# Performance work log

Hardware: AMD Instinct MI355X
Metric: run time of the kernel (lower is better)

Reference implementation:

```python
import jax, jax.numpy as jnp
import numpy as np

L, H, T, C, OUT, B = 8, 16, 2048, 1024, 1024, 4
DH = C // H
EPS = 1e-5


def _sincos_pos_embed(embed_dim, n):
    omega = np.arange(embed_dim // 2, dtype=np.float64) / (embed_dim / 2.0)
    omega = 1.0 / 10000 ** omega
    out = np.einsum('m,d->md', np.arange(n, dtype=np.float64), omega)
    return np.concatenate([np.sin(out), np.cos(out)], axis=1).astype(np.float32)


def setup_inputs() -> dict:
    key = jax.random.key(0)
    ks = jax.random.split(key, 12)
    s = 0.02  # torch init std
    n = lambda k, sh: jax.random.normal(k, sh, jnp.float32) * s
    zc = jnp.zeros((L, C), jnp.float32)
    return {
        'seq': jax.random.normal(ks[0], (B, T, C), jnp.float32),
        'pos_embed': jnp.asarray(_sincos_pos_embed(C, T))[None],  # [1,T,C]
        'Wq': n(ks[1], (L, C, C)), 'bq': zc,
        'Wk': n(ks[2], (L, C, C)), 'bk': zc,
        'Wv': n(ks[3], (L, C, C)), 'bv': zc,
        'Wo': n(ks[4], (L, C, C)), 'bo': zc,
        'ln1_w': jnp.ones((L, C), jnp.float32), 'ln1_b': zc,
        'ln2_w': jnp.ones((L, C), jnp.float32), 'ln2_b': zc,
        'W1': n(ks[5], (L, 4 * C, C)), 'b1': jnp.zeros((L, 4 * C), jnp.float32),
        'W2': n(ks[6], (L, C, 4 * C)), 'b2': zc,
        'lnf_w': jnp.ones((C,), jnp.float32), 'lnf_b': jnp.zeros((C,), jnp.float32),
        'Whead': n(ks[7], (OUT, C)),
    }


def _ln(x, w, b):
    mu = jnp.mean(x, -1, keepdims=True)
    var = jnp.mean(jnp.square(x - mu), -1, keepdims=True)
    return (x - mu) * jax.lax.rsqrt(var + EPS) * w + b


def _block(x, p):
    (Wq, bq, Wk, bk, Wv, bv, Wo, bo, l1w, l1b, l2w, l2b, W1, b1, W2, b2) = p
    b_, t_, c_ = x.shape
    h = _ln(x, l1w, l1b)
    q = (h @ Wq.T + bq).reshape(b_, t_, H, DH)
    k = (h @ Wk.T + bk).reshape(b_, t_, H, DH)
    v = (h @ Wv.T + bv).reshape(b_, t_, H, DH)
    # NOTE: source mask buffer is all ones -> no masking (full softmax)
    att = jnp.einsum('bqhd,bkhd->bhqk', q, k) * (1.0 / np.sqrt(DH))
    att = jax.nn.softmax(att, axis=-1)
    y = jnp.einsum('bhqk,bkhd->bqhd', att, v).reshape(b_, t_, c_)
    x = x + y @ Wo.T + bo
    h2 = _ln(x, l2w, l2b)
    x = x + jax.nn.gelu(h2 @ W1.T + b1, approximate=False) @ W2.T + b2
    return x, None


def reference(seq, pos_embed, Wq, bq, Wk, bk, Wv, bv, Wo, bo,
              ln1_w, ln1_b, ln2_w, ln2_b, W1, b1, W2, b2,
              lnf_w, lnf_b, Whead):
    t = seq.shape[1]
    x = seq + pos_embed[:, -t:, :]  # embedding dropout is identity at eval
    params = (Wq, bq, Wk, bk, Wv, bv, Wo, bo, ln1_w, ln1_b, ln2_w, ln2_b, W1, b1, W2, b2)
    x, _ = jax.lax.scan(_block, x, params)
    x = _ln(x, lnf_w, lnf_b)
    return x @ Whead.T
```

## Files before the change

kernel.cpp:

```cpp
#include <hip/hip_runtime.h>
#include <hip/hip_bf16.h>


#define LAYERS 8
#define NH 16
#define TT 2048
#define CC 1024
#define NB 4
#define MR (NB*TT)
#define LN_EPS 1e-5f

typedef __bf16 bf16_t;
typedef __attribute__((ext_vector_type(8))) __bf16 bf16x8;
typedef __attribute__((ext_vector_type(4))) __bf16 bf16x4;
typedef __attribute__((ext_vector_type(4))) float f32x4;
typedef __attribute__((ext_vector_type(8))) short s16x8;

__device__ inline f32x4 mfma16x16x32(bf16x8 a, bf16x8 b, f32x4 c) {
    return __builtin_amdgcn_mfma_f32_16x16x32_bf16(a, b, c, 0, 0, 0);
}

__device__ inline void gload_lds16(const void* g, void* lds) {
    __builtin_amdgcn_global_load_lds((const __attribute__((address_space(1))) void*)g,
                                     (__attribute__((address_space(3))) void*)lds, 16, 0, 0);
}


__global__ __launch_bounds__(256) void add_pos_k(const float* __restrict__ s,
                                                 const float* __restrict__ p,
                                                 float* __restrict__ x) {
    int i = blockIdx.x * 256 + threadIdx.x;
    float4 a = ((const float4*)s)[i];
    float4 b = ((const float4*)p)[i & ((TT * CC / 4) - 1)];
    ((float4*)x)[i] = make_float4(a.x + b.x, a.y + b.y, a.z + b.z, a.w + b.w);
}

__global__ __launch_bounds__(256) void f32_to_bf16_k(const float* __restrict__ s,
                                                     bf16_t* __restrict__ d, int n4) {
    int i = blockIdx.x * 256 + threadIdx.x;
    if (i < n4) {
        float4 v = ((const float4*)s)[i];
        bf16x4 o;
        o[0] = (bf16_t)v.x; o[1] = (bf16_t)v.y; o[2] = (bf16_t)v.z; o[3] = (bf16_t)v.w;
        ((bf16x4*)d)[i] = o;
    }
}

__global__ __launch_bounds__(256) void convert_layer_k(
        const float* __restrict__ Wq, const float* __restrict__ Wk,
        const float* __restrict__ Wv, const float* __restrict__ Wo,
        const float* __restrict__ W1, const float* __restrict__ W2,
        const float* __restrict__ bq, const float* __restrict__ bk,
        const float* __restrict__ bv,
        bf16_t* __restrict__ wqkvb, bf16_t* __restrict__ wob,
        bf16_t* __restrict__ w1b, bf16_t* __restrict__ w2b,
        float* __restrict__ bqkv) {
    const int i = blockIdx.x * 256 + threadIdx.x;
    if (i < 3145728) {
        const float4* s4;
        bf16_t* dst;
        int off;
        if (i < 262144)       { s4 = (const float4*)Wq + i;             dst = wqkvb; off = i; }
        else if (i < 524288)  { s4 = (const float4*)Wk + (i - 262144);  dst = wqkvb; off = i; }
        else if (i < 786432)  { s4 = (const float4*)Wv + (i - 524288);  dst = wqkvb; off = i; }
        else if (i < 1048576) { s4 = (const float4*)Wo + (i - 786432);  dst = wob;   off = i - 786432; }
        else if (i < 2097152) { s4 = (const float4*)W1 + (i - 1048576); dst = w1b;   off = i - 1048576; }
        else                  { s4 = (const float4*)W2 + (i - 2097152); dst = w2b;   off = i - 2097152; }
        float4 v = *s4;
        bf16x4 o;
        o[0] = (bf16_t)v.x; o[1] = (bf16_t)v.y; o[2] = (bf16_t)v.z; o[3] = (bf16_t)v.w;
        ((bf16x4*)dst)[off] = o;
    } else if (i < 3146496) {
        const int j = i - 3145728;
        const float* b = (j < 256) ? bq : (j < 512 ? bk : bv);
        ((float4*)bqkv)[j] = ((const float4*)b)[j & 255];
    }
}


__global__ __launch_bounds__(256) void ln_rows_k(const float* __restrict__ x,
                                                 const float* __restrict__ wgt,
                                                 const float* __restrict__ bgt,
                                                 bf16_t* __restrict__ out) {
    const int row = blockIdx.x * 4 + (threadIdx.x >> 6);
    const int l = threadIdx.x & 63;
    const float* xr = x + (size_t)row * CC;
    float4 v[4];
    float s = 0.f, sq = 0.f;
#pragma unroll
    for (int j = 0; j < 4; j++) {
        v[j] = *(const float4*)&xr[j * 256 + l * 4];
        s  += v[j].x + v[j].y + v[j].z + v[j].w;
        sq += v[j].x * v[j].x + v[j].y * v[j].y + v[j].z * v[j].z + v[j].w * v[j].w;
    }
#pragma unroll
    for (int m = 1; m < 64; m <<= 1) { s += __shfl_xor(s, m); sq += __shfl_xor(sq, m); }
    const float mu = s * (1.f / CC);
    const float rstd = rsqrtf(sq * (1.f / CC) - mu * mu + LN_EPS);
#pragma unroll
    for (int j = 0; j < 4; j++) {
        const int c0 = j * 256 + l * 4;
        const float4 wv = *(const float4*)&wgt[c0];
        const float4 bv = *(const float4*)&bgt[c0];
        bf16x4 o;
        o[0] = (bf16_t)((v[j].x - mu) * rstd * wv.x + bv.x);
        o[1] = (bf16_t)((v[j].y - mu) * rstd * wv.y + bv.y);
        o[2] = (bf16_t)((v[j].z - mu) * rstd * wv.z + bv.z);
        o[3] = (bf16_t)((v[j].w - mu) * rstd * wv.w + bv.w);
        *(bf16x4*)&out[(size_t)row * CC + c0] = o;
    }
}


#define EPI_BF16 0
#define EPI_GELU 1
#define EPI_RES  2
#define EPI_F32  3

template <int EPI>
__global__ __launch_bounds__(256) void gemm_bt(const bf16_t* __restrict__ A,
                                               const bf16_t* __restrict__ Bw,
                                               const float* __restrict__ bias,
                                               float* __restrict__ resid,
                                               bf16_t* __restrict__ obf,
                                               float* __restrict__ of32,
                                               int N, int K, int nbn) {
    __shared__ __align__(16) bf16_t As[128 * 32];
    __shared__ __align__(16) bf16_t Bs[128 * 32];
    const int nwg = gridDim.x;
    const int id = blockIdx.x;
    const int swz = (id & 7) * (nwg >> 3) + (id >> 3);
    const int bn = swz % nbn, bm = swz / nbn;
    const int t = threadIdx.x, w = t >> 6, l = t & 63;
    const int wm = (w >> 1) << 6, wn = (w & 1) << 6;
    const int fr = l & 15, fg = l >> 4;
    const int srow = l >> 2, scol = (l & 3) * 8;
    f32x4 acc[4][4] = {};
    for (int k0 = 0; k0 < K; k0 += 32) {
#pragma unroll
        for (int it = 0; it < 2; ++it) {
            const int rr = it * 64 + w * 16;
            gload_lds16(A  + (size_t)(bm * 128 + rr + srow) * K + k0 + scol, &As[rr * 32]);
            gload_lds16(Bw + (size_t)(bn * 128 + rr + srow) * K + k0 + scol, &Bs[rr * 32]);
        }
        __syncthreads();
        bf16x8 af[4], bfv[4];
#pragma unroll
        for (int i = 0; i < 4; i++) af[i]  = *(const bf16x8*)&As[(wm + i * 16 + fr) * 32 + fg * 8];
#pragma unroll
        for (int j = 0; j < 4; j++) bfv[j] = *(const bf16x8*)&Bs[(wn + j * 16 + fr) * 32 + fg * 8];
#pragma unroll
        for (int i = 0; i < 4; i++)
#pragma unroll
            for (int j = 0; j < 4; j++)
                acc[i][j] = mfma16x16x32(af[i], bfv[j], acc[i][j]);
        __syncthreads();
    }
#pragma unroll
    for (int i = 0; i < 4; i++) {
#pragma unroll
        for (int j = 0; j < 4; j++) {
            const int col = bn * 128 + wn + j * 16 + fr;
            float bv = 0.f;
            if constexpr (EPI != EPI_F32) bv = bias[col];
#pragma unroll
            for (int rg = 0; rg < 4; ++rg) {
                const int row = bm * 128 + wm + i * 16 + fg * 4 + rg;
                float v = acc[i][j][rg] + bv;
                if constexpr (EPI == EPI_BF16) {
                    obf[(size_t)row * N + col] = (bf16_t)v;
                } else if constexpr (EPI == EPI_GELU) {
                    v = 0.5f * v * (1.0f + erff(v * 0.70710678118f));
                    obf[(size_t)row * N + col] = (bf16_t)v;
                } else if constexpr (EPI == EPI_RES) {
                    resid[(size_t)row * CC + col] += v;
                } else {
                    of32[(size_t)row * N + col] = v;
                }
            }
        }
    }
}


__global__ __launch_bounds__(256, 2) void attn_k(const bf16_t* __restrict__ qkv,
                                                 bf16_t* __restrict__ y) {
    __shared__ __align__(16) bf16_t Ks[64 * 64];
    __shared__ __align__(16) bf16_t Vt[64 * 64];
    __shared__ __align__(16) bf16_t Ps[4 * 16 * 64];
    const int id = blockIdx.x;
    const int swz = (id & 7) * 256 + (id >> 3);
    const int qt = swz & 31, bh = swz >> 5;
    const int b = bh >> 4, h = bh & 15;
    const int t = threadIdx.x, w = t >> 6, l = t & 63;
    const int fr = l & 15, fg = l >> 4;
    const int q0 = qt * 64 + w * 16;
    const size_t bT = (size_t)b * TT;
    const float c2 = 0.125f * 1.44269504f;

    bf16x8 qf[2];
    {
        const size_t qoff = (bT + q0 + fr) * 3072 + h * 64 + fg * 8;
        qf[0] = *(const bf16x8*)&qkv[qoff];
        qf[1] = *(const bf16x8*)&qkv[qoff + 32];
    }
    float m[4] = {-1e30f, -1e30f, -1e30f, -1e30f};
    float lse[4] = {0.f, 0.f, 0.f, 0.f};
    f32x4 oacc[4] = {};

    const int srow = t >> 2;
    const int c8a = (t & 3) * 8;
    const int ksw = (srow & 7) << 4;
    char* KsB = (char*)Ks;
    char* VtB = (char*)Vt;
    char* PsB = (char*)Ps + w * 2048;

    s16x8 kr0, kr1, vr0, vr1;
    auto preload = [&](int kv0) {
        const size_t roff = (bT + kv0 + srow) * 3072 + h * 64;
        kr0 = *(const s16x8*)&qkv[roff + 1024 + c8a];
        kr1 = *(const s16x8*)&qkv[roff + 1024 + c8a + 32];
        vr0 = *(const s16x8*)&qkv[roff + 2048 + c8a];
        vr1 = *(const s16x8*)&qkv[roff + 2048 + c8a + 32];
    };
    preload(0);

    for (int kv0 = 0; kv0 < TT; kv0 += 64) {
        __syncthreads();
#pragma unroll
        for (int half = 0; half < 2; ++half) {
            const s16x8 kr = half ? kr1 : kr0;
            const s16x8 vr = half ? vr1 : vr0;
            const int c8 = c8a + half * 32;
            *(s16x8*)(KsB + srow * 128 + ((c8 * 2) ^ ksw)) = kr;
#pragma unroll
            for (int j = 0; j < 8; j++) {
                const int d = c8 + j;
                const int dsw = (((d & 7) ^ ((d >> 3) & 7)) << 4);
                *(short*)(VtB + d * 128 + ((srow * 2) ^ dsw)) = vr[j];
            }
        }
        __syncthreads();
        if (kv0 + 64 < TT) preload(kv0 + 64);

        f32x4 sacc[4] = {};
#pragma unroll
        for (int nt = 0; nt < 4; nt++) {
            const int kr_ = nt * 16 + fr;
            const int sw = (kr_ & 7) << 4;
#pragma unroll
            for (int c = 0; c < 2; c++) {
                bf16x8 kf = *(const bf16x8*)(KsB + kr_ * 128 + ((c * 64 + fg * 16) ^ sw));
                sacc[nt] = mfma16x16x32(qf[c], kf, sacc[nt]);
            }
        }
        float tm2[4];
#pragma unroll
        for (int rg = 0; rg < 4; rg++) {
            float tm = fmaxf(fmaxf(sacc[0][rg], sacc[1][rg]), fmaxf(sacc[2][rg], sacc[3][rg]));
            tm = fmaxf(tm, __shfl_xor(tm, 1));
            tm = fmaxf(tm, __shfl_xor(tm, 2));
            tm = fmaxf(tm, __shfl_xor(tm, 4));
            tm = fmaxf(tm, __shfl_xor(tm, 8));
            tm2[rg] = tm * c2;
        }
        const float need = fmaxf(fmaxf(tm2[0] - m[0], tm2[1] - m[1]),
                                 fmaxf(tm2[2] - m[2], tm2[3] - m[3]));
        if (!__all(need <= 11.5f)) {
#pragma unroll
            for (int rg = 0; rg < 4; rg++) {
                const float mn = fmaxf(m[rg], tm2[rg]);
                const float co = exp2f(m[rg] - mn);
                lse[rg] *= co;
                m[rg] = mn;
#pragma unroll
                for (int nd = 0; nd < 4; nd++) oacc[nd][rg] *= co;
            }
        }
        float pv[4][4];
#pragma unroll
        for (int rg = 0; rg < 4; rg++) {
            float rs = 0.f;
#pragma unroll
            for (int nt = 0; nt < 4; nt++) {
                const float p = exp2f(sacc[nt][rg] * c2 - m[rg]);
                pv[nt][rg] = p;
                rs += p;
            }
            rs += __shfl_xor(rs, 1);
            rs += __shfl_xor(rs, 2);
            rs += __shfl_xor(rs, 4);
            rs += __shfl_xor(rs, 8);
            lse[rg] += rs;
        }
#pragma unroll
        for (int nt = 0; nt < 4; nt++) {
#pragma unroll
            for (int rg = 0; rg < 4; rg++) {
                const int pr_ = fg * 4 + rg;
                *(bf16_t*)(PsB + pr_ * 128 + ((nt * 32 + fr * 2) ^ ((pr_ & 7) << 4))) =
                    (bf16_t)pv[nt][rg];
            }
        }
        bf16x8 pf[2];
        {
            const int sw = (fr & 7) << 4;
            pf[0] = *(const bf16x8*)(PsB + fr * 128 + ((fg * 16) ^ sw));
            pf[1] = *(const bf16x8*)(PsB + fr * 128 + ((64 + fg * 16) ^ sw));
        }
#pragma unroll
        for (int nd = 0; nd < 4; nd++) {
            const int dr = nd * 16 + fr;
            const int dsw = (((dr & 7) ^ ((dr >> 3) & 7)) << 4);
#pragma unroll
            for (int c = 0; c < 2; c++) {
                bf16x8 vf = *(const bf16x8*)(VtB + dr * 128 + ((c * 64 + fg * 16) ^ dsw));
                oacc[nd] = mfma16x16x32(pf[c], vf, oacc[nd]);
            }
        }
    }
#pragma unroll
    for (int rg = 0; rg < 4; rg++) {
        const float inv = 1.f / lse[rg];
        const size_t ro = (bT + q0 + fg * 4 + rg) * CC + h * 64;
#pragma unroll
        for (int nd = 0; nd < 4; nd++)
            y[ro + nd * 16 + fr] = (bf16_t)(oacc[nd][rg] * inv);
    }
}


extern "C" void kernel_launch(void* const* d_in, const int* in_sizes, int n_in,
                              void* d_out, int out_size, void* d_ws, size_t ws_size,
                              hipStream_t stream) {
    (void)in_sizes; (void)n_in; (void)out_size; (void)ws_size;
    const float* seq  = (const float*)d_in[0];
    const float* pos  = (const float*)d_in[1];
    const float* Wq   = (const float*)d_in[2];
    const float* bq   = (const float*)d_in[3];
    const float* Wk   = (const float*)d_in[4];
    const float* bk   = (const float*)d_in[5];
    const float* Wv   = (const float*)d_in[6];
    const float* bv   = (const float*)d_in[7];
    const float* Wo   = (const float*)d_in[8];
    const float* bo   = (const float*)d_in[9];
    const float* ln1w = (const float*)d_in[10];
    const float* ln1b = (const float*)d_in[11];
    const float* ln2w = (const float*)d_in[12];
    const float* ln2b = (const float*)d_in[13];
    const float* W1   = (const float*)d_in[14];
    const float* b1   = (const float*)d_in[15];
    const float* W2   = (const float*)d_in[16];
    const float* b2   = (const float*)d_in[17];
    const float* lnfw = (const float*)d_in[18];
    const float* lnfb = (const float*)d_in[19];
    const float* Wh   = (const float*)d_in[20];
    float* out = (float*)d_out;

    char* ws = (char*)d_ws;
    float*  x     = (float*)(ws + 0);
    bf16_t* qkvb  = (bf16_t*)(ws + 33554432);
    bf16_t* yb    = (bf16_t*)(ws + 83886080);
    bf16_t* a1b   = (bf16_t*)(ws + 33554432);
    bf16_t* hb    = (bf16_t*)(ws + 100663296);
    bf16_t* wqkvb = (bf16_t*)(ws + 117440512);
    bf16_t* wob   = (bf16_t*)(ws + 123731968);
    bf16_t* w1b   = (bf16_t*)(ws + 125829120);
    bf16_t* w2b   = (bf16_t*)(ws + 134217728);
    bf16_t* whb   = (bf16_t*)(ws + 142606336);
    float*  bqkv  = (float*)(ws + 144703488);

    f32_to_bf16_k<<<1024, 256, 0, stream>>>(Wh, whb, 262144);
    add_pos_k<<<8192, 256, 0, stream>>>(seq, pos, x);

    for (int l = 0; l < LAYERS; ++l) {
        const size_t wo_ = (size_t)l * CC * CC;
        const size_t w4_ = (size_t)l * 4 * CC * CC;
        convert_layer_k<<<12291, 256, 0, stream>>>(Wq + wo_, Wk + wo_, Wv + wo_, Wo + wo_,
                                                   W1 + w4_, W2 + w4_,
                                                   bq + l * CC, bk + l * CC, bv + l * CC,
                                                   wqkvb, wob, w1b, w2b, bqkv);

        ln_rows_k<<<2048, 256, 0, stream>>>(x, ln1w + l * CC, ln1b + l * CC, hb);
        gemm_bt<EPI_BF16><<<1536, 256, 0, stream>>>(hb, wqkvb, bqkv, nullptr,
                                                    qkvb, nullptr, 3072, 1024, 24);
        attn_k<<<2048, 256, 0, stream>>>(qkvb, yb);
        gemm_bt<EPI_RES><<<512, 256, 0, stream>>>(yb, wob, bo + l * CC, x,
                                                  nullptr, nullptr, 1024, 1024, 8);
        ln_rows_k<<<2048, 256, 0, stream>>>(x, ln2w + l * CC, ln2b + l * CC, hb);
        gemm_bt<EPI_GELU><<<2048, 256, 0, stream>>>(hb, w1b, b1 + (size_t)l * 4 * CC,
                                                    nullptr, a1b, nullptr, 4096, 1024, 32);
        gemm_bt<EPI_RES><<<512, 256, 0, stream>>>(a1b, w2b, b2 + l * CC, x,
                                                  nullptr, nullptr, 1024, 4096, 8);
    }
    ln_rows_k<<<2048, 256, 0, stream>>>(x, lnfw, lnfb, hb);
    gemm_bt<EPI_F32><<<512, 256, 0, stream>>>(hb, whb, nullptr, nullptr,
                                              nullptr, out, 1024, 1024, 8);
}
```

Baseline: 5.027 ms.

## Keep attention P in registers via transposed QK^T and lane shuffles

The attention kernel now computes S transposed (K as the A operand), so each lane holds the scores for a single query row. Row max and sum then need only two cross-lane shuffles, and the softmax state shrinks to one scalar per lane. The P tile is packed to bf16 and rearranged into the PV MFMA operand layout with register shuffles instead of a round trip through shared memory, which removes the Ps buffer. Occupancy is raised to 4 blocks per CU, which tightens register limits and risks spills.

```diff
diff --git a/kernel.cpp b/kernel.cpp
--- a/kernel.cpp
+++ b/kernel.cpp
@@ -15,6 +15,7 @@
 typedef __attribute__((ext_vector_type(4))) __bf16 bf16x4;
 typedef __attribute__((ext_vector_type(4))) float f32x4;
 typedef __attribute__((ext_vector_type(8))) short s16x8;
+typedef __attribute__((ext_vector_type(4))) unsigned u32x4;
 
 __device__ inline f32x4 mfma16x16x32(bf16x8 a, bf16x8 b, f32x4 c) {
     return __builtin_amdgcn_mfma_f32_16x16x32_bf16(a, b, c, 0, 0, 0);
@@ -23,6 +24,12 @@
 __device__ inline void gload_lds16(const void* g, void* lds) {
     __builtin_amdgcn_global_load_lds((const __attribute__((address_space(1))) void*)g,
                                      (__attribute__((address_space(3))) void*)lds, 16, 0, 0);
+}
+
+__device__ inline unsigned pack_bf16(float a, float b) {
+    unsigned short ua = __builtin_bit_cast(unsigned short, (bf16_t)a);
+    unsigned short ub = __builtin_bit_cast(unsigned short, (bf16_t)b);
+    return (unsigned)ua | ((unsigned)ub << 16);
 }
 
 
@@ -183,20 +190,20 @@
 }
 
 
-__global__ __launch_bounds__(256, 2) void attn_k(const bf16_t* __restrict__ qkv,
+__global__ __launch_bounds__(256, 4) void attn_k(const bf16_t* __restrict__ qkv,
                                                  bf16_t* __restrict__ y) {
     __shared__ __align__(16) bf16_t Ks[64 * 64];
     __shared__ __align__(16) bf16_t Vt[64 * 64];
-    __shared__ __align__(16) bf16_t Ps[4 * 16 * 64];
     const int id = blockIdx.x;
     const int swz = (id & 7) * 256 + (id >> 3);
     const int qt = swz & 31, bh = swz >> 5;
     const int b = bh >> 4, h = bh & 15;
     const int t = threadIdx.x, w = t >> 6, l = t & 63;
     const int fr = l & 15, fg = l >> 4;
+    const int hh = fg >> 1;
     const int q0 = qt * 64 + w * 16;
     const size_t bT = (size_t)b * TT;
-    const float c2 = 0.125f * 1.44269504f;
+    const float SCL = 0.125f * 1.44269504f;
 
     bf16x8 qf[2];
     {
@@ -204,8 +211,7 @@
         qf[0] = *(const bf16x8*)&qkv[qoff];
         qf[1] = *(const bf16x8*)&qkv[qoff + 32];
     }
-    float m[4] = {-1e30f, -1e30f, -1e30f, -1e30f};
-    float lse[4] = {0.f, 0.f, 0.f, 0.f};
+    float mrun = -1e30f, lse = 0.f;
     f32x4 oacc[4] = {};
 
     const int srow = t >> 2;
@@ -213,7 +219,6 @@
     const int ksw = (srow & 7) << 4;
     char* KsB = (char*)Ks;
     char* VtB = (char*)Vt;
-    char* PsB = (char*)Ps + w * 2048;
 
     s16x8 kr0, kr1, vr0, vr1;
     auto preload = [&](int kv0) {
@@ -251,81 +256,92 @@
 #pragma unroll
             for (int c = 0; c < 2; c++) {
                 bf16x8 kf = *(const bf16x8*)(KsB + kr_ * 128 + ((c * 64 + fg * 16) ^ sw));
-                sacc[nt] = mfma16x16x32(qf[c], kf, sacc[nt]);
+                sacc[nt] = mfma16x16x32(kf, qf[c], sacc[nt]);
             }
         }
-        float tm2[4];
+        float tm = sacc[0][0];
+#pragma unroll
+        for (int nt = 0; nt < 4; nt++)
+#pragma unroll
+            for (int rg = 0; rg < 4; rg++) tm = fmaxf(tm, sacc[nt][rg]);
+        tm = fmaxf(tm, __shfl_xor(tm, 16));
+        tm = fmaxf(tm, __shfl_xor(tm, 32));
+        tm *= SCL;
+        if (!__all(tm - mrun <= 11.5f)) {
+            const float mn = fmaxf(mrun, tm);
+            const float co = exp2f(mrun - mn);
+            lse *= co; mrun = mn;
+            const float cr0 = __shfl(co, fg * 4 + 0);
+            const float cr1 = __shfl(co, fg * 4 + 1);
+            const float cr2 = __shfl(co, fg * 4 + 2);
+            const float cr3 = __shfl(co, fg * 4 + 3);
+#pragma unroll
+            for (int nd = 0; nd < 4; nd++) {
+                oacc[nd][0] *= cr0; oacc[nd][1] *= cr1;
+                oacc[nd][2] *= cr2; oacc[nd][3] *= cr3;
+            }
+        }
+        const f32x4 sA0 = hh ? sacc[1] : sacc[0];
+        const f32x4 sA1 = hh ? sacc[3] : sacc[2];
+        const f32x4 sB0 = hh ? sacc[0] : sacc[1];
+        const f32x4 sB1 = hh ? sacc[2] : sacc[3];
+        float rs = 0.f;
+        unsigned pkA[4], pkB[4];
 #pragma unroll
         for (int rg = 0; rg < 4; rg++) {
-            float tm = fmaxf(fmaxf(sacc[0][rg], sacc[1][rg]), fmaxf(sacc[2][rg], sacc[3][rg]));
-            tm = fmaxf(tm, __shfl_xor(tm, 1));
-            tm = fmaxf(tm, __shfl_xor(tm, 2));
-            tm = fmaxf(tm, __shfl_xor(tm, 4));
-            tm = fmaxf(tm, __shfl_xor(tm, 8));
-            tm2[rg] = tm * c2;
-        }
-        const float need = fmaxf(fmaxf(tm2[0] - m[0], tm2[1] - m[1]),
-                                 fmaxf(tm2[2] - m[2], tm2[3] - m[3]));
-        if (!__all(need <= 11.5f)) {
-#pragma unroll
-            for (int rg = 0; rg < 4; rg++) {
-                const float mn = fmaxf(m[rg], tm2[rg]);
-                const float co = exp2f(m[rg] - mn);
-                lse[rg] *= co;
-                m[rg] = mn;
-#pragma unroll
-                for (int nd = 0; nd < 4; nd++) oacc[nd][rg] *= co;
-            }
-        }
-        float pv[4][4];
+            const float a0 = exp2f(sA0[rg] * SCL - mrun);
+            const float a1 = exp2f(sA1[rg] * SCL - mrun);
+            const float b0 = exp2f(sB0[rg] * SCL - mrun);
+            const float b1 = exp2f(sB1[rg] * SCL - mrun);
+            rs += (a0 + a1) + (b0 + b1);
+            pkA[rg] = pack_bf16(a0, a1);
+            pkB[rg] = pack_bf16(b0, b1);
+        }
+        rs += __shfl_xor(rs, 16);
+        rs += __shfl_xor(rs, 32);
+        lse += rs;
+        unsigned s0pk[4], s1pk[4];
 #pragma unroll
         for (int rg = 0; rg < 4; rg++) {
-            float rs = 0.f;
-#pragma unroll
-            for (int nt = 0; nt < 4; nt++) {
-                const float p = exp2f(sacc[nt][rg] * c2 - m[rg]);
-                pv[nt][rg] = p;
-                rs += p;
-            }
-            rs += __shfl_xor(rs, 1);
-            rs += __shfl_xor(rs, 2);
-            rs += __shfl_xor(rs, 4);
-            rs += __shfl_xor(rs, 8);
-            lse[rg] += rs;
-        }
-#pragma unroll
-        for (int nt = 0; nt < 4; nt++) {
-#pragma unroll
-            for (int rg = 0; rg < 4; rg++) {
-                const int pr_ = fg * 4 + rg;
-                *(bf16_t*)(PsB + pr_ * 128 + ((nt * 32 + fr * 2) ^ ((pr_ & 7) << 4))) =
-                    (bf16_t)pv[nt][rg];
-            }
-        }
-        bf16x8 pf[2];
-        {
-            const int sw = (fr & 7) << 4;
-            pf[0] = *(const bf16x8*)(PsB + fr * 128 + ((fg * 16) ^ sw));
-            pf[1] = *(const bf16x8*)(PsB + fr * 128 + ((64 + fg * 16) ^ sw));
-        }
+            const unsigned r16 = __shfl_xor(pkA[rg], 16);
+            const unsigned r32 = __shfl_xor(pkB[rg], 32);
+            const unsigned r48 = __shfl_xor(pkB[rg], 48);
+            s0pk[rg] = (fg == 0) ? pkA[rg] : (fg == 1) ? r48 : (fg == 2) ? r32 : r16;
+            s1pk[rg] = (fg == 0) ? r16 : (fg == 1) ? r32 : (fg == 2) ? r48 : pkA[rg];
+        }
+        u32x4 w0v, w1v;
+        w0v[0] = (s0pk[0] & 0xFFFFu) | (s0pk[1] << 16);
+        w0v[1] = (s0pk[2] & 0xFFFFu) | (s0pk[3] << 16);
+        w0v[2] = (s1pk[0] & 0xFFFFu) | (s1pk[1] << 16);
+        w0v[3] = (s1pk[2] & 0xFFFFu) | (s1pk[3] << 16);
+        w1v[0] = (s0pk[0] >> 16) | (s0pk[1] & 0xFFFF0000u);
+        w1v[1] = (s0pk[2] >> 16) | (s0pk[3] & 0xFFFF0000u);
+        w1v[2] = (s1pk[0] >> 16) | (s1pk[1] & 0xFFFF0000u);
+        w1v[3] = (s1pk[2] >> 16) | (s1pk[3] & 0xFFFF0000u);
+        const bf16x8 paf0 = __builtin_bit_cast(bf16x8, w0v);
+        const bf16x8 paf1 = __builtin_bit_cast(bf16x8, w1v);
 #pragma unroll
         for (int nd = 0; nd < 4; nd++) {
             const int dr = nd * 16 + fr;
             const int dsw = (((dr & 7) ^ ((dr >> 3) & 7)) << 4);
-#pragma unroll
-            for (int c = 0; c < 2; c++) {
-                bf16x8 vf = *(const bf16x8*)(VtB + dr * 128 + ((c * 64 + fg * 16) ^ dsw));
-                oacc[nd] = mfma16x16x32(pf[c], vf, oacc[nd]);
-            }
-        }
-    }
-#pragma unroll
-    for (int rg = 0; rg < 4; rg++) {
-        const float inv = 1.f / lse[rg];
-        const size_t ro = (bT + q0 + fg * 4 + rg) * CC + h * 64;
-#pragma unroll
-        for (int nd = 0; nd < 4; nd++)
-            y[ro + nd * 16 + fr] = (bf16_t)(oacc[nd][rg] * inv);
+            bf16x8 vf0 = *(const bf16x8*)(VtB + dr * 128 + ((fg * 16) ^ dsw));
+            oacc[nd] = mfma16x16x32(paf0, vf0, oacc[nd]);
+            bf16x8 vf1 = *(const bf16x8*)(VtB + dr * 128 + ((64 + fg * 16) ^ dsw));
+            oacc[nd] = mfma16x16x32(paf1, vf1, oacc[nd]);
+        }
+    }
+    const float inv = 1.f / lse;
+    const float i0 = __shfl(inv, fg * 4 + 0);
+    const float i1 = __shfl(inv, fg * 4 + 1);
+    const float i2 = __shfl(inv, fg * 4 + 2);
+    const float i3 = __shfl(inv, fg * 4 + 3);
+#pragma unroll
+    for (int nd = 0; nd < 4; nd++) {
+        const size_t ro = (bT + q0 + fg * 4) * CC + h * 64 + nd * 16 + fr;
+        y[ro]          = (bf16_t)(oacc[nd][0] * i0);
+        y[ro + CC]     = (bf16_t)(oacc[nd][1] * i1);
+        y[ro + 2 * CC] = (bf16_t)(oacc[nd][2] * i2);
+        y[ro + 3 * CC] = (bf16_t)(oacc[nd][3] * i3);
     }
 }
 
```

After: 4.620 ms. 1.09x faster.
